# Optimization experiments

Hardware: AMD Instinct MI355X
Metric: run time of the kernel (lower is better)

The kernel has to match this reference:

```python
import jax, jax.numpy as jnp
import numpy as np

NH = 8          # num_heads
EMB = 256       # embed_dim
HD = EMB // NH  # head_dim
NV = 6          # num_views
NL = 4          # num_fmap_levels
NP = 4          # num_ref_points
NZ = 4          # num_z_ref_points
OFFSET_SCALE = 1.0
SHAPES = [(64, 64), (32, 32), (16, 16), (8, 8)]
SLEN = sum(h * w for h, w in SHAPES)  # 5440


def setup_inputs() -> dict:
    key = jax.random.key(0)
    ks = jax.random.split(key, 9)
    N, Q = 1, 1600
    A = NH * NV * NL * NP * NZ  # total sampling slots per query
    s = 0.02
    return {
        "queries": jax.random.normal(ks[0], (N, Q, EMB), jnp.float32),
        # pre-normalized reference points in [-1, 1] (normalize_ref_points=False path)
        "ref_points": jax.random.uniform(ks[1], (N, Q, NV, NL, NZ, 2), jnp.float32, -1.0, 1.0),
        "value": jax.random.normal(ks[2], (N, NV, SLEN, EMB), jnp.float32),
        "value_spatial_shapes": jnp.asarray(SHAPES, jnp.int32),
        "Wv": jax.random.normal(ks[3], (EMB, EMB), jnp.float32) * s,
        "Woff": jax.random.normal(ks[4], (A * 2, EMB), jnp.float32) * s,
        "boff": jnp.zeros((A * 2,), jnp.float32),
        "Wattn": jax.random.normal(ks[5], (A, EMB), jnp.float32) * s,
        "battn": jnp.zeros((A,), jnp.float32),
        "Wout": jax.random.normal(ks[6], (EMB, EMB), jnp.float32) * s,
    }


def _forward(queries, ref_points, value, shapes_np, Wv, Woff, boff, Wattn, battn, Wout):
    N, Q, C = queries.shape
    # sampling offsets: tanh-bounded, scaled
    offs = jnp.tanh(queries @ Woff.T + boff) * OFFSET_SCALE
    offs = offs.reshape(N, Q, NH, NV, NL, NP, NZ, 2)
    # attention weights: softmax over all (view, level, point, z) slots per head
    attn = (queries @ Wattn.T + battn).reshape(N, Q, NH, NV * NL * NP * NZ)
    attn = jax.nn.softmax(attn, axis=-1).reshape(N, Q, NH, NV, NL, NP, NZ)
    # value projection, split heads: (N, V, H, S, hd)
    val = (value @ Wv.T).reshape(N, NV, -1, NH, HD)
    val = jnp.transpose(val, (0, 1, 3, 2, 4))
    # sampling locations, clamped to [-1, 1] (grid_sample normalized coords)
    locs = jnp.clip(ref_points[:, :, None, :, :, None, :, :] + offs, -1.0, 1.0)  # (N,Q,H,V,L,P,Z,2)
    locs = jnp.transpose(locs, (0, 3, 2, 4, 1, 5, 6, 7))   # (N,V,H,L,Q,P,Z,2)
    attn_t = jnp.transpose(attn, (0, 3, 2, 4, 1, 5, 6))     # (N,V,H,L,Q,P,Z)

    out = jnp.zeros((N, Q, NH, HD), queries.dtype)
    start = 0
    for l in range(NL):
        Hl, Wl = int(shapes_np[l, 0]), int(shapes_np[l, 1])
        S = Hl * Wl
        fmap = val[:, :, :, start:start + S, :]  # (N,V,H,S,hd)
        g = locs[:, :, :, l].reshape(N, NV, NH, Q * NP * NZ, 2)
        # align_corners=True mapping; coords are clamped so zero-padding never triggers
        x = (g[..., 0] + 1.0) * 0.5 * (Wl - 1)
        y = (g[..., 1] + 1.0) * 0.5 * (Hl - 1)
        x0 = jnp.floor(x); y0 = jnp.floor(y)
        wx = x - x0; wy = y - y0
        x0i = jnp.clip(x0.astype(jnp.int32), 0, Wl - 1)
        y0i = jnp.clip(y0.astype(jnp.int32), 0, Hl - 1)
        x1i = jnp.clip(x0i + 1, 0, Wl - 1)
        y1i = jnp.clip(y0i + 1, 0, Hl - 1)

        def gat(yi, xi):
            return jnp.take_along_axis(fmap, (yi * Wl + xi)[..., None], axis=3)

        samp = (((1 - wy) * (1 - wx))[..., None] * gat(y0i, x0i)
                + ((1 - wy) * wx)[..., None] * gat(y0i, x1i)
                + (wy * (1 - wx))[..., None] * gat(y1i, x0i)
                + (wy * wx)[..., None] * gat(y1i, x1i))  # (N,V,H,QPZ,hd)
        samp = samp.reshape(N, NV, NH, Q, NP, NZ, HD)
        out = out + jnp.einsum('nvhqpzd,nvhqpz->nqhd', samp, attn_t[:, :, :, l])
        start += S

    out = out.reshape(N, Q, C)
    return out @ Wout.T  # out_fc (dropout is identity at inference)


def reference(queries, ref_points, value, value_spatial_shapes, Wv, Woff, boff, Wattn, battn, Wout):
    shapes_np = np.asarray(value_spatial_shapes)
    return _forward(queries, ref_points, value, shapes_np, Wv, Woff, boff, Wattn, battn, Wout)
```

## Files before the change

kernel.cpp:

```cpp
#include <hip/hip_runtime.h>
#include <hip/hip_bf16.h>
#include <math.h>

#define NHh   8
#define EMB   256
#define HDd   32
#define NVv   6
#define SLENs 5440
#define QQ    1600
#define A_ATTN 3072
#define A_OFF  6144

typedef _Float16 half8 __attribute__((ext_vector_type(8)));
typedef __attribute__((ext_vector_type(4))) float f32x4;

__device__ __forceinline__ unsigned short f2bf(float f) {
  __hip_bfloat16 h = __float2bfloat16(f);
  return *(unsigned short*)&h;
}
__device__ __forceinline__ unsigned short f2h(float f) {
  _Float16 h = (_Float16)f;
  return __builtin_bit_cast(unsigned short, h);
}
__device__ __forceinline__ float h2f(unsigned short u) {
  return (float)__builtin_bit_cast(_Float16, u);
}

__device__ __forceinline__ void dma16(const unsigned short* g, unsigned short* l) {
  __builtin_amdgcn_global_load_lds(
      (const __attribute__((address_space(1))) unsigned int*)g,
      (__attribute__((address_space(3))) unsigned int*)l, 16, 0, 0);
}

__global__ __launch_bounds__(256) void split_h_kernel(
    const float* __restrict__ q, const float* __restrict__ value,
    const float* __restrict__ Woff, const float* __restrict__ Wattn,
    const float* __restrict__ Wv, const float* __restrict__ Wout,
    unsigned short* __restrict__ q16, unsigned short* __restrict__ v16,
    unsigned short* __restrict__ Wq16, unsigned short* __restrict__ Wv16,
    unsigned short* __restrict__ Wout16) {
  int i4 = blockIdx.x * 256 + threadIdx.x;
  const float* src; unsigned short* dst; int loc;
  if      (i4 < 102400)  { src = q;     dst = q16;    loc = i4; }
  else if (i4 < 2191360) { src = value; dst = v16;    loc = i4 - 102400; }
  else if (i4 < 2584576) { src = Woff;  dst = Wq16;   loc = i4 - 2191360; }
  else if (i4 < 2781184) { src = Wattn; dst = Wq16;   loc = i4 - 2584576 + 393216; }
  else if (i4 < 2797568) { src = Wv;    dst = Wv16;   loc = i4 - 2781184; }
  else                   { src = Wout;  dst = Wout16; loc = i4 - 2797568; }
  float4 x = ((const float4*)src)[loc - (src == Woff ? 0 : 0)];
  if (src == Wattn) x = ((const float4*)src)[loc - 393216];
  ushort4 hh;
  hh.x = f2h(x.x); hh.y = f2h(x.y); hh.z = f2h(x.z); hh.w = f2h(x.w);
  ((ushort4*)dst)[loc] = hh;
}

template <int MODE>
__global__ __launch_bounds__(256) void gemmh_kernel(
    const unsigned short* __restrict__ Ah, const unsigned short* __restrict__ Bh,
    const float* __restrict__ bias, const float* __restrict__ bias2,
    void* __restrict__ Cv, void* __restrict__ Cv2,
    int M, int N, int K) {
  __shared__ unsigned short LAh[128 * 32], LBh[128 * 32];

  const int tid = threadIdx.x;
  const int bm = blockIdx.y * 128, bn = blockIdx.x * 128;
  const int lane = tid & 63, w = tid >> 6;
  const int wm = (w & 1) * 64, wn = (w >> 1) * 64;
  const int l16 = lane & 15, quad = lane >> 4;

  const int c0 = tid, c1 = tid + 256;
  const int r0 = c0 >> 2, s0 = (c0 & 3) * 8;
  const int r1 = c1 >> 2, s1 = (c1 & 3) * 8;
  const size_t a0 = (size_t)min(bm + r0, M - 1) * K + s0;
  const size_t a1 = (size_t)min(bm + r1, M - 1) * K + s1;
  const size_t b0o = (size_t)(bn + r0) * K + s0;
  const size_t b1o = (size_t)(bn + r1) * K + s1;
  const int l0 = c0 * 8, l1 = c1 * 8;

  f32x4 acc[4][4] = {};

  for (int k0 = 0; k0 < K; k0 += 32) {
    dma16(&Ah[a0 + k0], &LAh[l0]);
    dma16(&Ah[a1 + k0], &LAh[l1]);
    dma16(&Bh[b0o + k0], &LBh[l0]);
    dma16(&Bh[b1o + k0], &LBh[l1]);
    __syncthreads();

    half8 fa[4], fb[4];
#pragma unroll
    for (int i = 0; i < 4; ++i) {
      int ar = (wm + i * 16 + l16) * 32 + quad * 8;
      int br = (wn + i * 16 + l16) * 32 + quad * 8;
      fa[i] = *(const half8*)&LAh[ar];
      fb[i] = *(const half8*)&LBh[br];
    }
#pragma unroll
    for (int i = 0; i < 4; ++i)
#pragma unroll
      for (int j = 0; j < 4; ++j)
        acc[i][j] = __builtin_amdgcn_mfma_f32_16x16x32_f16(fa[i], fb[j], acc[i][j], 0, 0, 0);
    __syncthreads();
  }

#pragma unroll
  for (int j = 0; j < 4; ++j) {
    int n = bn + wn + j * 16 + l16;
    float bv = 0.f;
    bool dotanh = false;
    if (MODE == 3) {
      if (n < A_OFF) { bv = bias[n]; dotanh = true; }
      else bv = bias2[n - A_OFF];
    } else if (MODE == 0) {
      if (bias) bv = bias[n];
    }
#pragma unroll
    for (int i = 0; i < 4; ++i) {
      int mbase = bm + wm + i * 16 + quad * 4;
#pragma unroll
      for (int reg = 0; reg < 4; ++reg) {
        int m = mbase + reg;
        if (m >= M) continue;
        float c = acc[i][j][reg] + bv;
        if (MODE == 3) {
          if (dotanh) {
            float t = __expf(2.f * c);
            c = 1.f - 2.f / (t + 1.f);
            ((unsigned short*)Cv)[(size_t)m * A_OFF + n] = f2h(c);
          } else {
            ((unsigned short*)Cv2)[(size_t)m * A_ATTN + (n - A_OFF)] = f2h(c);
          }
        } else if (MODE == 2) {
          int vv = m / SLENs;
          int s = m - vv * SLENs;
          int hh2 = n >> 5, dd = n & 31;
          ((unsigned short*)Cv)[((size_t)(vv * 8 + hh2) * SLENs + s) * 32 + dd] = f2bf(c);
        } else {
          ((float*)Cv)[(size_t)m * N + n] = c;
        }
      }
    }
  }
}

__global__ __launch_bounds__(256) void sample_kernel(
    const float* __restrict__ ref, const unsigned short* __restrict__ offs16,
    const unsigned short* __restrict__ attn16,
    const unsigned short* __restrict__ val_t,
    unsigned short* __restrict__ op16) {
  __shared__ int   Lrb[4][384];
  __shared__ uint2 Lrw[4][384];

  const int h   = blockIdx.x & 7;
  const int qt  = blockIdx.x >> 3;
  const int wid = threadIdx.x >> 6;
  const int lane = threadIdx.x & 63;
  const int q   = qt * 4 + wid;
  const int row = q * 8 + h;

  {
    const unsigned short* ap = attn16 + (size_t)row * 384;
    float vals[6];
    float mx = -1e30f;
#pragma unroll
    for (int i = 0; i < 6; ++i) { vals[i] = h2f(ap[lane + i * 64]); mx = fmaxf(mx, vals[i]); }
#pragma unroll
    for (int o = 32; o > 0; o >>= 1) mx = fmaxf(mx, __shfl_xor(mx, o, 64));
    float s = 0.f;
#pragma unroll
    for (int i = 0; i < 6; ++i) { vals[i] = __expf(vals[i] - mx); s += vals[i]; }
#pragma unroll
    for (int o = 32; o > 0; o >>= 1) s += __shfl_xor(s, o, 64);
    const float inv = 1.0f / s;

    const int l = (lane >> 4) & 3;
    const int z = lane & 3;
    const int Wl = 64 >> l;
    const int start = (l == 0) ? 0 : (l == 1 ? 4096 : (l == 2 ? 5120 : 5376));
    const float sc = 0.5f * (float)(Wl - 1);
    const unsigned int* op = (const unsigned int*)offs16 + (size_t)row * 384;
    const float* rq = ref + (size_t)q * (NVv * 4 * 4 * 2);

#pragma unroll 1
    for (int v = 0; v < 6; ++v) {
      int j = v * 64 + lane;
      float w = vals[v] * inv;
      unsigned int oxy = op[j];
      float ox = h2f((unsigned short)(oxy & 0xFFFF));
      float oy = h2f((unsigned short)(oxy >> 16));
      const float* rp = rq + ((v * 4 + l) * 4 + z) * 2;
      float rx = rp[0], ry = rp[1];
      float x = fminf(1.f, fmaxf(-1.f, rx + ox));
      float y = fminf(1.f, fmaxf(-1.f, ry + oy));
      float xp = (x + 1.f) * sc, yp = (y + 1.f) * sc;
      float x0f = floorf(xp), y0f = floorf(yp);
      int x0 = (int)x0f, y0 = (int)y0f;
      float wx = xp - x0f, wy = yp - y0f;
      int fx = (x0 + 1 < Wl) ? 1 : 0;
      int fy = (y0 + 1 < Wl) ? 2 : 0;
      float wxw = wx * w, wmx = w - wxw;
      float w01 = wxw * (1.f - wy), w11 = wxw * wy;
      float w00 = wmx * (1.f - wy), w10 = wmx * wy;
      Lrb[wid][j] = ((start + y0 * Wl + x0) << 6) | fx | fy;
      Lrw[wid][j] = make_uint2(((unsigned)f2bf(w01) << 16) | f2bf(w00),
                               ((unsigned)f2bf(w11) << 16) | f2bf(w10));
    }
  }

  const int e16 = (lane & 3) << 4;
  const int cxm = ((lane >> 2) & 1) << 6;
  const bool cy = (lane >> 3) & 1;
  const int r   = lane >> 4;

  float acc[8] = {};
  int ib = r;

#pragma unroll 1
  for (int v = 0; v < 6; ++v) {
    const char* sb = (const char*)val_t + (size_t)(v * 8 + h) * (SLENs * 64);
#pragma unroll 1
    for (int l = 0; l < 4; ++l) {
      const int cym = cy ? (2 << (11 - l)) : 0;
#pragma unroll
      for (int i = 0; i < 4; ++i) {
        int ri = ib + i * 4;
        int bf = Lrb[wid][ri];
        uint2 pk2 = Lrw[wid][ri];
        int voff = ((bf & -64) | e16) + ((bf << 6) & cxm) + ((bf << (11 - l)) & cym);
        uint4 u = *(const uint4*)(sb + voff);
        unsigned int pk = cy ? pk2.y : pk2.x;
        float wl_ = __uint_as_float(cxm ? (pk & 0xFFFF0000u) : (pk << 16));
        acc[0] = fmaf(wl_, __uint_as_float(u.x << 16),          acc[0]);
        acc[1] = fmaf(wl_, __uint_as_float(u.x & 0xFFFF0000u),  acc[1]);
        acc[2] = fmaf(wl_, __uint_as_float(u.y << 16),          acc[2]);
        acc[3] = fmaf(wl_, __uint_as_float(u.y & 0xFFFF0000u),  acc[3]);
        acc[4] = fmaf(wl_, __uint_as_float(u.z << 16),          acc[4]);
        acc[5] = fmaf(wl_, __uint_as_float(u.z & 0xFFFF0000u),  acc[5]);
        acc[6] = fmaf(wl_, __uint_as_float(u.w << 16),          acc[6]);
        acc[7] = fmaf(wl_, __uint_as_float(u.w & 0xFFFF0000u),  acc[7]);
      }
      ib += 16;
    }
  }

#pragma unroll
  for (int m = 4; m <= 32; m <<= 1)
#pragma unroll
    for (int j = 0; j < 8; ++j) acc[j] += __shfl_xor(acc[j], m, 64);

  if (lane < 4) {
    int off = q * EMB + h * 32 + lane * 8;
    ushort4 h0, h1;
    h0.x = f2h(acc[0]); h0.y = f2h(acc[1]); h0.z = f2h(acc[2]); h0.w = f2h(acc[3]);
    h1.x = f2h(acc[4]); h1.y = f2h(acc[5]); h1.z = f2h(acc[6]); h1.w = f2h(acc[7]);
    *(ushort4*)&op16[off] = h0;  *(ushort4*)&op16[off + 4] = h1;
  }
}

extern "C" void kernel_launch(void* const* d_in, const int* in_sizes, int n_in,
                              void* d_out, int out_size, void* d_ws, size_t ws_size,
                              hipStream_t stream) {
  const float* queries    = (const float*)d_in[0];
  const float* ref_points = (const float*)d_in[1];
  const float* value      = (const float*)d_in[2];
  const float* Wv    = (const float*)d_in[4];
  const float* Woff  = (const float*)d_in[5];
  const float* boff  = (const float*)d_in[6];
  const float* Wattn = (const float*)d_in[7];
  const float* battn = (const float*)d_in[8];
  const float* Wout  = (const float*)d_in[9];
  float* out = (float*)d_out;

  char* W = (char*)d_ws;
  unsigned short* offs16 = (unsigned short*)(W + 0);
  unsigned short* attn16 = (unsigned short*)(W + 19660800);
  unsigned short* val_t  = (unsigned short*)(W + 29491200);
  unsigned short* q16    = (unsigned short*)(W + 46202880);
  unsigned short* v16    = (unsigned short*)(W + 47022080);
  unsigned short* Wq16   = (unsigned short*)(W + 63733760);
  unsigned short* Wv16   = (unsigned short*)(W + 68452352);
  unsigned short* Wout16 = (unsigned short*)(W + 68583424);
  unsigned short* op16   = (unsigned short*)(W + 68714496);

  dim3 blk(256);

  split_h_kernel<<<10992, blk, 0, stream>>>(
      queries, value, Woff, Wattn, Wv, Wout, q16, v16, Wq16, Wv16, Wout16);
  gemmh_kernel<3><<<dim3(9216 / 128, (QQ + 127) / 128), blk, 0, stream>>>(
      q16, Wq16, boff, battn, offs16, attn16, QQ, 9216, EMB);
  gemmh_kernel<2><<<dim3(EMB / 128, (NVv * SLENs) / 128), blk, 0, stream>>>(
      v16, Wv16, nullptr, nullptr, val_t, nullptr, NVv * SLENs, EMB, EMB);
  sample_kernel<<<QQ * NHh / 4, blk, 0, stream>>>(
      ref_points, offs16, attn16, val_t, op16);
  gemmh_kernel<0><<<dim3(EMB / 128, (QQ + 127) / 128), blk, 0, stream>>>(
      op16, Wout16, nullptr, nullptr, out, nullptr, QQ, EMB, EMB);
}
```

Before: 238.5 us.

## Merge query and value projection GEMMs into one launch; precompute bilinear corner offsets

The query-projection GEMM (offsets and attention logits) and the value-projection GEMM now run as one kernel launch. Block indices are split between the two problems, so both fill the GPU together and one launch is saved. The sampling kernel now stores all four bilinear corner byte offsets per sample in shared memory. This removes the per-lane bit-masking address arithmetic in the gather loop and flattens the level loop into one partially unrolled loop. In exchange it uses more LDS per block (int4 instead of int), which could reduce occupancy, and the merged GEMM kernel carries branchy epilogue code.

```diff
diff --git a/kernel.cpp b/kernel.cpp
--- a/kernel.cpp
+++ b/kernel.cpp
@@ -40,30 +40,42 @@
     unsigned short* __restrict__ Wq16, unsigned short* __restrict__ Wv16,
     unsigned short* __restrict__ Wout16) {
   int i4 = blockIdx.x * 256 + threadIdx.x;
-  const float* src; unsigned short* dst; int loc;
-  if      (i4 < 102400)  { src = q;     dst = q16;    loc = i4; }
-  else if (i4 < 2191360) { src = value; dst = v16;    loc = i4 - 102400; }
-  else if (i4 < 2584576) { src = Woff;  dst = Wq16;   loc = i4 - 2191360; }
-  else if (i4 < 2781184) { src = Wattn; dst = Wq16;   loc = i4 - 2584576 + 393216; }
-  else if (i4 < 2797568) { src = Wv;    dst = Wv16;   loc = i4 - 2781184; }
-  else                   { src = Wout;  dst = Wout16; loc = i4 - 2797568; }
-  float4 x = ((const float4*)src)[loc - (src == Woff ? 0 : 0)];
-  if (src == Wattn) x = ((const float4*)src)[loc - 393216];
+  const float* src; unsigned short* dst; int sloc; int dloc;
+  if      (i4 < 102400)  { src = q;     dst = q16;    sloc = i4;           dloc = sloc; }
+  else if (i4 < 2191360) { src = value; dst = v16;    sloc = i4 - 102400;  dloc = sloc; }
+  else if (i4 < 2584576) { src = Woff;  dst = Wq16;   sloc = i4 - 2191360; dloc = sloc; }
+  else if (i4 < 2781184) { src = Wattn; dst = Wq16;   sloc = i4 - 2584576; dloc = sloc + 393216; }
+  else if (i4 < 2797568) { src = Wv;    dst = Wv16;   sloc = i4 - 2781184; dloc = sloc; }
+  else                   { src = Wout;  dst = Wout16; sloc = i4 - 2797568; dloc = sloc; }
+  float4 x = ((const float4*)src)[sloc];
   ushort4 hh;
   hh.x = f2h(x.x); hh.y = f2h(x.y); hh.z = f2h(x.z); hh.w = f2h(x.w);
-  ((ushort4*)dst)[loc] = hh;
-}
-
-template <int MODE>
-__global__ __launch_bounds__(256) void gemmh_kernel(
-    const unsigned short* __restrict__ Ah, const unsigned short* __restrict__ Bh,
-    const float* __restrict__ bias, const float* __restrict__ bias2,
-    void* __restrict__ Cv, void* __restrict__ Cv2,
-    int M, int N, int K) {
+  ((ushort4*)dst)[dloc] = hh;
+}
+
+__global__ __launch_bounds__(256) void gemm23_kernel(
+    const unsigned short* __restrict__ q16, const unsigned short* __restrict__ Wq16,
+    const unsigned short* __restrict__ v16, const unsigned short* __restrict__ Wv16,
+    const float* __restrict__ boff, const float* __restrict__ battn,
+    unsigned short* __restrict__ offs16, unsigned short* __restrict__ attn16,
+    unsigned short* __restrict__ val_t) {
   __shared__ unsigned short LAh[128 * 32], LBh[128 * 32];
 
+  const int bid = blockIdx.x;
+  const unsigned short *A, *B;
+  int M, bm, bn;
+  bool isVal;
+  if (bid < 936) {
+    A = q16;  B = Wq16;  M = QQ;
+    bn = (bid % 72) * 128;  bm = (bid / 72) * 128;  isVal = false;
+  } else {
+    int b2 = bid - 936;
+    A = v16;  B = Wv16;  M = NVv * SLENs;
+    bn = (b2 & 1) * 128;  bm = (b2 >> 1) * 128;  isVal = true;
+  }
+  const int K = EMB;
+
   const int tid = threadIdx.x;
-  const int bm = blockIdx.y * 128, bn = blockIdx.x * 128;
   const int lane = tid & 63, w = tid >> 6;
   const int wm = (w & 1) * 64, wn = (w >> 1) * 64;
   const int l16 = lane & 15, quad = lane >> 4;
@@ -80,6 +92,85 @@
   f32x4 acc[4][4] = {};
 
   for (int k0 = 0; k0 < K; k0 += 32) {
+    dma16(&A[a0 + k0], &LAh[l0]);
+    dma16(&A[a1 + k0], &LAh[l1]);
+    dma16(&B[b0o + k0], &LBh[l0]);
+    dma16(&B[b1o + k0], &LBh[l1]);
+    __syncthreads();
+
+    half8 fa[4], fb[4];
+#pragma unroll
+    for (int i = 0; i < 4; ++i) {
+      int ar = (wm + i * 16 + l16) * 32 + quad * 8;
+      int br = (wn + i * 16 + l16) * 32 + quad * 8;
+      fa[i] = *(const half8*)&LAh[ar];
+      fb[i] = *(const half8*)&LBh[br];
+    }
+#pragma unroll
+    for (int i = 0; i < 4; ++i)
+#pragma unroll
+      for (int j = 0; j < 4; ++j)
+        acc[i][j] = __builtin_amdgcn_mfma_f32_16x16x32_f16(fa[i], fb[j], acc[i][j], 0, 0, 0);
+    __syncthreads();
+  }
+
+#pragma unroll
+  for (int j = 0; j < 4; ++j) {
+    int n = bn + wn + j * 16 + l16;
+    float bv = 0.f;
+    bool dotanh = false;
+    if (!isVal) {
+      if (n < A_OFF) { bv = boff[n]; dotanh = true; }
+      else bv = battn[n - A_OFF];
+    }
+#pragma unroll
+    for (int i = 0; i < 4; ++i) {
+      int mbase = bm + wm + i * 16 + quad * 4;
+#pragma unroll
+      for (int reg = 0; reg < 4; ++reg) {
+        int m = mbase + reg;
+        if (m >= M) continue;
+        float c = acc[i][j][reg] + bv;
+        if (isVal) {
+          int vv = m / SLENs;
+          int s = m - vv * SLENs;
+          int hh2 = n >> 5, dd = n & 31;
+          val_t[((size_t)(vv * 8 + hh2) * SLENs + s) * 32 + dd] = f2bf(c);
+        } else if (dotanh) {
+          float t = __expf(2.f * c);
+          c = 1.f - 2.f / (t + 1.f);
+          offs16[(size_t)m * A_OFF + n] = f2h(c);
+        } else {
+          attn16[(size_t)m * A_ATTN + (n - A_OFF)] = f2h(c);
+        }
+      }
+    }
+  }
+}
+
+__global__ __launch_bounds__(256) void gemmh0_kernel(
+    const unsigned short* __restrict__ Ah, const unsigned short* __restrict__ Bh,
+    float* __restrict__ C, int M, int N, int K) {
+  __shared__ unsigned short LAh[128 * 32], LBh[128 * 32];
+
+  const int tid = threadIdx.x;
+  const int bm = blockIdx.y * 128, bn = blockIdx.x * 128;
+  const int lane = tid & 63, w = tid >> 6;
+  const int wm = (w & 1) * 64, wn = (w >> 1) * 64;
+  const int l16 = lane & 15, quad = lane >> 4;
+
+  const int c0 = tid, c1 = tid + 256;
+  const int r0 = c0 >> 2, s0 = (c0 & 3) * 8;
+  const int r1 = c1 >> 2, s1 = (c1 & 3) * 8;
+  const size_t a0 = (size_t)min(bm + r0, M - 1) * K + s0;
+  const size_t a1 = (size_t)min(bm + r1, M - 1) * K + s1;
+  const size_t b0o = (size_t)(bn + r0) * K + s0;
+  const size_t b1o = (size_t)(bn + r1) * K + s1;
+  const int l0 = c0 * 8, l1 = c1 * 8;
+
+  f32x4 acc[4][4] = {};
+
+  for (int k0 = 0; k0 < K; k0 += 32) {
     dma16(&Ah[a0 + k0], &LAh[l0]);
     dma16(&Ah[a1 + k0], &LAh[l1]);
     dma16(&Bh[b0o + k0], &LBh[l0]);
@@ -105,14 +196,6 @@
 #pragma unroll
   for (int j = 0; j < 4; ++j) {
     int n = bn + wn + j * 16 + l16;
-    float bv = 0.f;
-    bool dotanh = false;
-    if (MODE == 3) {
-      if (n < A_OFF) { bv = bias[n]; dotanh = true; }
-      else bv = bias2[n - A_OFF];
-    } else if (MODE == 0) {
-      if (bias) bv = bias[n];
-    }
 #pragma unroll
     for (int i = 0; i < 4; ++i) {
       int mbase = bm + wm + i * 16 + quad * 4;
@@ -120,23 +203,7 @@
       for (int reg = 0; reg < 4; ++reg) {
         int m = mbase + reg;
         if (m >= M) continue;
-        float c = acc[i][j][reg] + bv;
-        if (MODE == 3) {
-          if (dotanh) {
-            float t = __expf(2.f * c);
-            c = 1.f - 2.f / (t + 1.f);
-            ((unsigned short*)Cv)[(size_t)m * A_OFF + n] = f2h(c);
-          } else {
-            ((unsigned short*)Cv2)[(size_t)m * A_ATTN + (n - A_OFF)] = f2h(c);
-          }
-        } else if (MODE == 2) {
-          int vv = m / SLENs;
-          int s = m - vv * SLENs;
-          int hh2 = n >> 5, dd = n & 31;
-          ((unsigned short*)Cv)[((size_t)(vv * 8 + hh2) * SLENs + s) * 32 + dd] = f2bf(c);
-        } else {
-          ((float*)Cv)[(size_t)m * N + n] = c;
-        }
+        C[(size_t)m * N + n] = acc[i][j][reg];
       }
     }
   }
@@ -147,7 +214,7 @@
     const unsigned short* __restrict__ attn16,
     const unsigned short* __restrict__ val_t,
     unsigned short* __restrict__ op16) {
-  __shared__ int   Lrb[4][384];
+  __shared__ int4  Lco[4][384];
   __shared__ uint2 Lrw[4][384];
 
   const int h   = blockIdx.x & 7;
@@ -176,6 +243,7 @@
     const int z = lane & 3;
     const int Wl = 64 >> l;
     const int start = (l == 0) ? 0 : (l == 1 ? 4096 : (l == 2 ? 5120 : 5376));
+    const int strideB = 4096 >> l;
     const float sc = 0.5f * (float)(Wl - 1);
     const unsigned int* op = (const unsigned int*)offs16 + (size_t)row * 384;
     const float* rq = ref + (size_t)q * (NVv * 4 * 4 * 2);
@@ -195,50 +263,45 @@
       float x0f = floorf(xp), y0f = floorf(yp);
       int x0 = (int)x0f, y0 = (int)y0f;
       float wx = xp - x0f, wy = yp - y0f;
-      int fx = (x0 + 1 < Wl) ? 1 : 0;
-      int fy = (y0 + 1 < Wl) ? 2 : 0;
+      int b0 = (start + y0 * Wl + x0) << 6;
+      int dx = (x0 + 1 < Wl) ? 64 : 0;
+      int dy = (y0 + 1 < Wl) ? strideB : 0;
       float wxw = wx * w, wmx = w - wxw;
       float w01 = wxw * (1.f - wy), w11 = wxw * wy;
       float w00 = wmx * (1.f - wy), w10 = wmx * wy;
-      Lrb[wid][j] = ((start + y0 * Wl + x0) << 6) | fx | fy;
+      Lco[wid][j] = make_int4(b0, b0 + dx, b0 + dy, b0 + dx + dy);
       Lrw[wid][j] = make_uint2(((unsigned)f2bf(w01) << 16) | f2bf(w00),
                                ((unsigned)f2bf(w11) << 16) | f2bf(w10));
     }
   }
 
+  const int cb  = (lane >> 2) & 3;
   const int e16 = (lane & 3) << 4;
-  const int cxm = ((lane >> 2) & 1) << 6;
-  const bool cy = (lane >> 3) & 1;
   const int r   = lane >> 4;
 
+  const int* LcoW = (const int*)&Lco[wid][0];
+  const unsigned short* LrwW = (const unsigned short*)&Lrw[wid][0];
+
   float acc[8] = {};
-  int ib = r;
 
 #pragma unroll 1
   for (int v = 0; v < 6; ++v) {
     const char* sb = (const char*)val_t + (size_t)(v * 8 + h) * (SLENs * 64);
-#pragma unroll 1
-    for (int l = 0; l < 4; ++l) {
-      const int cym = cy ? (2 << (11 - l)) : 0;
-#pragma unroll
-      for (int i = 0; i < 4; ++i) {
-        int ri = ib + i * 4;
-        int bf = Lrb[wid][ri];
-        uint2 pk2 = Lrw[wid][ri];
-        int voff = ((bf & -64) | e16) + ((bf << 6) & cxm) + ((bf << (11 - l)) & cym);
-        uint4 u = *(const uint4*)(sb + voff);
-        unsigned int pk = cy ? pk2.y : pk2.x;
-        float wl_ = __uint_as_float(cxm ? (pk & 0xFFFF0000u) : (pk << 16));
-        acc[0] = fmaf(wl_, __uint_as_float(u.x << 16),          acc[0]);
-        acc[1] = fmaf(wl_, __uint_as_float(u.x & 0xFFFF0000u),  acc[1]);
-        acc[2] = fmaf(wl_, __uint_as_float(u.y << 16),          acc[2]);
-        acc[3] = fmaf(wl_, __uint_as_float(u.y & 0xFFFF0000u),  acc[3]);
-        acc[4] = fmaf(wl_, __uint_as_float(u.z << 16),          acc[4]);
-        acc[5] = fmaf(wl_, __uint_as_float(u.z & 0xFFFF0000u),  acc[5]);
-        acc[6] = fmaf(wl_, __uint_as_float(u.w << 16),          acc[6]);
-        acc[7] = fmaf(wl_, __uint_as_float(u.w & 0xFFFF0000u),  acc[7]);
-      }
-      ib += 16;
+    const int rbase = v * 64 + r;
+#pragma unroll 4
+    for (int t = 0; t < 16; ++t) {
+      int ri = rbase + t * 4;
+      int off = LcoW[ri * 4 + cb];
+      float wl_ = __uint_as_float((unsigned int)LrwW[ri * 4 + cb] << 16);
+      uint4 u = *(const uint4*)(sb + (off + e16));
+      acc[0] = fmaf(wl_, __uint_as_float(u.x << 16),          acc[0]);
+      acc[1] = fmaf(wl_, __uint_as_float(u.x & 0xFFFF0000u),  acc[1]);
+      acc[2] = fmaf(wl_, __uint_as_float(u.y << 16),          acc[2]);
+      acc[3] = fmaf(wl_, __uint_as_float(u.y & 0xFFFF0000u),  acc[3]);
+      acc[4] = fmaf(wl_, __uint_as_float(u.z << 16),          acc[4]);
+      acc[5] = fmaf(wl_, __uint_as_float(u.z & 0xFFFF0000u),  acc[5]);
+      acc[6] = fmaf(wl_, __uint_as_float(u.w << 16),          acc[6]);
+      acc[7] = fmaf(wl_, __uint_as_float(u.w & 0xFFFF0000u),  acc[7]);
     }
   }
 
@@ -285,12 +348,10 @@
 
   split_h_kernel<<<10992, blk, 0, stream>>>(
       queries, value, Woff, Wattn, Wv, Wout, q16, v16, Wq16, Wv16, Wout16);
-  gemmh_kernel<3><<<dim3(9216 / 128, (QQ + 127) / 128), blk, 0, stream>>>(
-      q16, Wq16, boff, battn, offs16, attn16, QQ, 9216, EMB);
-  gemmh_kernel<2><<<dim3(EMB / 128, (NVv * SLENs) / 128), blk, 0, stream>>>(
-      v16, Wv16, nullptr, nullptr, val_t, nullptr, NVv * SLENs, EMB, EMB);
+  gemm23_kernel<<<1446, blk, 0, stream>>>(
+      q16, Wq16, v16, Wv16, boff, battn, offs16, attn16, val_t);
   sample_kernel<<<QQ * NHh / 4, blk, 0, stream>>>(
       ref_points, offs16, attn16, val_t, op16);
-  gemmh_kernel<0><<<dim3(EMB / 128, (QQ + 127) / 128), blk, 0, stream>>>(
-      op16, Wout16, nullptr, nullptr, out, nullptr, QQ, EMB, EMB);
-}
+  gemmh0_kernel<<<dim3(EMB / 128, (QQ + 127) / 128), blk, 0, stream>>>(
+      op16, Wout16, out, QQ, EMB, EMB);
+}
```

Result: faster. 210.6 us (-11.7%).
